# Kernel tuning notes

Hardware: AMD Instinct MI355X
Metric: run time of the kernel (lower is better)

## Reference

```python
import jax, jax.numpy as jnp
import numpy as np
import math

D = 1024
N_HEAD = 16
HEAD_D = D // N_HEAD

def setup_inputs() -> dict:
    key = jax.random.key(0)
    ks = jax.random.split(key, 10)
    b, s = 4, 2048
    scale = 1.0 / math.sqrt(D)
    inp = {
        "decoder_hs": jax.random.normal(ks[0], (b, s, D), dtype=jnp.float32),
        "encoder_hs": jax.random.normal(ks[1], (b, s, D), dtype=jnp.float32),
        "Wq": jax.random.normal(ks[2], (D, D), dtype=jnp.float32) * scale,
        "bq": jnp.zeros((D,), dtype=jnp.float32),
        "Wk": jax.random.normal(ks[3], (D, D), dtype=jnp.float32) * scale,
        "bk": jnp.zeros((D,), dtype=jnp.float32),
        "Wv": jax.random.normal(ks[4], (D, D), dtype=jnp.float32) * scale,
        "bv": jnp.zeros((D,), dtype=jnp.float32),
        "Wp": jax.random.normal(ks[5], (D, D), dtype=jnp.float32) * scale,
        "bp": jnp.zeros((D,), dtype=jnp.float32),
    }
    return inp

def _split_heads(x, b, s):
    # [b, s, d] -> [b, n_head, s, head_d]
    return x.reshape(b, s, N_HEAD, HEAD_D).transpose(0, 2, 1, 3)

def reference(decoder_hs, encoder_hs, Wq, bq, Wk, bk, Wv, bv, Wp, bp):
    b, s, d = decoder_hs.shape
    # torch nn.Linear: y = x @ W.T + b
    q = _split_heads(decoder_hs @ Wq.T + bq, b, s)
    k = _split_heads(encoder_hs @ Wk.T + bk, b, s)
    v = _split_heads(encoder_hs @ Wv.T + bv, b, s)
    att = jnp.einsum('bhqd,bhkd->bhqk', q, k) * (1.0 / math.sqrt(HEAD_D))
    att = jax.nn.softmax(att, axis=-1)  # mask is None, dropout = 0 (eval)
    y = jnp.einsum('bhqk,bhkd->bhqd', att, v)
    y = y.transpose(0, 2, 1, 3).reshape(b, s, d)
    return y @ Wp.T + bp
```

## Files before the change

kernel.cpp:

```cpp
#include <hip/hip_runtime.h>
#include <hip/hip_bf16.h>

typedef __attribute__((ext_vector_type(8))) short bf16x8;
typedef __attribute__((ext_vector_type(4))) float floatx4;
typedef __attribute__((ext_vector_type(16))) float floatx16;
typedef __attribute__((ext_vector_type(2))) int int2v;

#define MFMA_16x16x32(A, B, C) __builtin_amdgcn_mfma_f32_16x16x32_bf16(A, B, C, 0, 0, 0)
#define MFMA_32x32x16(A, B, C) __builtin_amdgcn_mfma_f32_32x32x16_bf16(A, B, C, 0, 0, 0)

__device__ __forceinline__ unsigned short f2b(float f) {
    __hip_bfloat16 h = __float2bfloat16(f);
    unsigned short u;
    __builtin_memcpy(&u, &h, 2);
    return u;
}
__device__ __forceinline__ unsigned pk2(float a, float b) {
    __hip_bfloat162 h = __float22bfloat162_rn(float2{a, b});
    unsigned u;
    __builtin_memcpy(&u, &h, 4);
    return u;
}
__device__ __forceinline__ bf16x8 mk8(int a, int b, int c, int d) {
    union { int u[4]; bf16x8 v; } x;
    x.u[0] = a; x.u[1] = b; x.u[2] = c; x.u[3] = d;
    return x.v;
}
__device__ __forceinline__ void async_lds16(const void* g, void* l) {
    __builtin_amdgcn_global_load_lds((__attribute__((address_space(1))) void*)g,
                                     (__attribute__((address_space(3))) void*)l, 16, 0, 0);
}

struct CvtArgs {
    const float* src[6];
    unsigned short* dst[6];
    float scale[6];
    int n8[6];
};
__global__ __launch_bounds__(256) void convert_kernel(CvtArgs a) {
    const int t = blockIdx.y;
    const int i = blockIdx.x * 256 + threadIdx.x;
    if (i >= a.n8[t]) return;
    const float sc = a.scale[t];
    const float4* s = (const float4*)a.src[t];
    const float4 x = s[2 * i], y = s[2 * i + 1];
    bf16x8 v;
    v[0] = (short)f2b(x.x * sc); v[1] = (short)f2b(x.y * sc);
    v[2] = (short)f2b(x.z * sc); v[3] = (short)f2b(x.w * sc);
    v[4] = (short)f2b(y.x * sc); v[5] = (short)f2b(y.y * sc);
    v[6] = (short)f2b(y.z * sc); v[7] = (short)f2b(y.w * sc);
    *(bf16x8*)(a.dst[t] + (size_t)i * 8) = v;
}

struct QKVArgs {
    const unsigned short* A[3];
    const unsigned short* B[3];
    const float* bias[3];
    float bscale[3];
    unsigned short* C[3];
};
__global__ __launch_bounds__(256, 4) void gemm_qkv(QKVArgs args) {
    constexpr int M = 8192, N = 1024, K = 1024;
    __shared__ __align__(16) unsigned short As[2][4096];
    __shared__ __align__(16) unsigned short Bs[2][4096];

    const int z = blockIdx.z;
    const unsigned short* __restrict__ A = args.A[z];
    const unsigned short* __restrict__ B = args.B[z];
    const float* __restrict__ bias = args.bias[z];
    const float bsc = args.bscale[z];
    unsigned short* __restrict__ C = args.C[z];

    const int tid  = threadIdx.x;
    const int wave = tid >> 6;
    const int lane = tid & 63;
    const int l16  = lane & 15;
    const int quad = lane >> 4;
    const int bm = (blockIdx.x & 63) * 128;
    const int bn = (blockIdx.x >> 6) * 128;
    const int wm = (wave >> 1) * 64;
    const int wn = (wave & 1) * 64;

    const int srow = tid >> 2;
    const int skb  = (((tid & 3) ^ ((tid >> 2) & 3) ^ ((tid >> 4) & 3)) * 8);
    const int cq   = ((quad ^ (l16 & 3) ^ ((l16 >> 2) & 3)) * 8);

    floatx4 acc[4][4] = {};

    auto stage = [&](int buf, int k0) {
        async_lds16(A + (size_t)(bm + srow) * K + skb + k0,      &As[buf][tid * 8]);
        async_lds16(A + (size_t)(bm + 64 + srow) * K + skb + k0, &As[buf][2048 + tid * 8]);
        async_lds16(B + (size_t)(bn + srow) * K + skb + k0,      &Bs[buf][tid * 8]);
        async_lds16(B + (size_t)(bn + 64 + srow) * K + skb + k0, &Bs[buf][2048 + tid * 8]);
    };

    stage(0, 0);
    for (int it = 0; it < K / 32; ++it) {
        __syncthreads();
        if (it + 1 < K / 32) stage((it + 1) & 1, (it + 1) * 32);
        const unsigned short* Ac = &As[it & 1][0];
        const unsigned short* Bc = &Bs[it & 1][0];

        bf16x8 af[4], bfr[4];
        #pragma unroll
        for (int i = 0; i < 4; ++i)
            af[i] = *(const bf16x8*)&Ac[(wm + i * 16 + l16) * 32 + cq];
        #pragma unroll
        for (int j = 0; j < 4; ++j)
            bfr[j] = *(const bf16x8*)&Bc[(wn + j * 16 + l16) * 32 + cq];
        #pragma unroll
        for (int i = 0; i < 4; ++i)
            #pragma unroll
            for (int j = 0; j < 4; ++j)
                acc[i][j] = MFMA_16x16x32(af[i], bfr[j], acc[i][j]);
    }

    if (z == 2) {
        #pragma unroll
        for (int j = 0; j < 4; ++j) {
            const int col = bn + wn + j * 16 + l16;
            const float bv = bias[col] * bsc;
            #pragma unroll
            for (int i = 0; i < 4; ++i) {
                uint2 w;
                w.x = pk2(acc[i][j][0] + bv, acc[i][j][1] + bv);
                w.y = pk2(acc[i][j][2] + bv, acc[i][j][3] + bv);
                const size_t off = (size_t)col * (size_t)M + (bm + wm + i * 16 + quad * 4);
                *(uint2*)&C[off] = w;
            }
        }
    } else {
        #pragma unroll
        for (int i = 0; i < 4; ++i) {
            const int row = bm + wm + i * 16 + quad * 4;
            #pragma unroll
            for (int j = 0; j < 4; ++j) {
                const int col = bn + wn + j * 16 + l16;
                const float bv = bias[col] * bsc;
                #pragma unroll
                for (int r = 0; r < 4; ++r)
                    C[(size_t)(row + r) * N + col] = f2b(acc[i][j][r] + bv);
            }
        }
    }
}

__global__ __launch_bounds__(256, 4) void gemm_out(
    const unsigned short* __restrict__ A, const unsigned short* __restrict__ B,
    const float* __restrict__ bias, float* __restrict__ C,
    int M, int N, int K)
{
    __shared__ __align__(16) unsigned short As[2][4096];
    __shared__ __align__(16) unsigned short Bs[2][4096];

    const int tid  = threadIdx.x;
    const int wave = tid >> 6;
    const int lane = tid & 63;
    const int l16  = lane & 15;
    const int quad = lane >> 4;
    const int bm = (blockIdx.x & 63) * 128;
    const int bn = (blockIdx.x >> 6) * 128;
    const int wm = (wave >> 1) * 64;
    const int wn = (wave & 1) * 64;

    const int srow = tid >> 2;
    const int skb  = (((tid & 3) ^ ((tid >> 2) & 3) ^ ((tid >> 4) & 3)) * 8);
    const int cq   = ((quad ^ (l16 & 3) ^ ((l16 >> 2) & 3)) * 8);

    floatx4 acc[4][4] = {};

    auto stage = [&](int buf, int k0) {
        async_lds16(A + (size_t)(bm + srow) * K + skb + k0,      &As[buf][tid * 8]);
        async_lds16(A + (size_t)(bm + 64 + srow) * K + skb + k0, &As[buf][2048 + tid * 8]);
        async_lds16(B + (size_t)(bn + srow) * K + skb + k0,      &Bs[buf][tid * 8]);
        async_lds16(B + (size_t)(bn + 64 + srow) * K + skb + k0, &Bs[buf][2048 + tid * 8]);
    };

    stage(0, 0);
    for (int it = 0; it < K / 32; ++it) {
        __syncthreads();
        if (it + 1 < K / 32) stage((it + 1) & 1, (it + 1) * 32);
        const unsigned short* Ac = &As[it & 1][0];
        const unsigned short* Bc = &Bs[it & 1][0];

        bf16x8 af[4], bfr[4];
        #pragma unroll
        for (int i = 0; i < 4; ++i)
            af[i] = *(const bf16x8*)&Ac[(wm + i * 16 + l16) * 32 + cq];
        #pragma unroll
        for (int j = 0; j < 4; ++j)
            bfr[j] = *(const bf16x8*)&Bc[(wn + j * 16 + l16) * 32 + cq];
        #pragma unroll
        for (int i = 0; i < 4; ++i)
            #pragma unroll
            for (int j = 0; j < 4; ++j)
                acc[i][j] = MFMA_16x16x32(af[i], bfr[j], acc[i][j]);
    }

    float* Tw = ((wave < 2) ? (float*)&As[0][0] : (float*)&Bs[0][0]) + (wave & 1) * 1024;
    const int rrow = lane >> 2;
    const int rch  = lane & 3;
    #pragma unroll
    for (int i = 0; i < 4; ++i) {
        #pragma unroll
        for (int j = 0; j < 4; ++j) {
            const int col = j * 16 + l16;
            const float bv = bias[bn + wn + col];
            floatx4 v;
            #pragma unroll
            for (int r = 0; r < 4; ++r) v[r] = acc[i][j][r] + bv;
            *(floatx4*)&Tw[col * 16 + ((quad ^ (col & 3)) << 2)] = v;
        }
        const int grow = bm + wm + i * 16 + rrow;
        #pragma unroll
        for (int k = 0; k < 4; ++k) {
            const int c0 = (rch + 4 * k) * 4;
            floatx4 v;
            #pragma unroll
            for (int c = 0; c < 4; ++c) {
                const int col = c0 + c;
                v[c] = Tw[col * 16 + ((((rrow >> 2) ^ col) & 3) << 2) + (rrow & 3)];
            }
            *(floatx4*)&C[(size_t)grow * N + bn + wn + c0] = v;
        }
    }
}

__global__ __launch_bounds__(256, 4) void attn_kernel(
    const unsigned short* __restrict__ Q, const unsigned short* __restrict__ Kg,
    const unsigned short* __restrict__ Vt, unsigned short* __restrict__ Y)
{
    __shared__ __align__(16) unsigned short Ks[2][4096];
    __shared__ __align__(16) unsigned short Vs[2][4096];

    const int tid  = threadIdx.x;
    const int wave = tid >> 6;
    const int lane = tid & 63;
    const int l31  = lane & 31;
    const int hi   = lane >> 5;
    const int x7   = lane & 7;
    const int h4   = ((lane >> 4) & 1) << 2;
    const int bh = blockIdx.x & 63;
    const int qt = blockIdx.x >> 6;
    const int b  = bh >> 4;
    const int h  = bh & 15;
    const int q0 = qt * 128 + wave * 32;
    const size_t base  = ((size_t)b * 2048) * 1024 + (size_t)h * 64;
    const size_t vbase = ((size_t)h * 64) * 8192 + (size_t)b * 2048;

    bf16x8 qf[4];
    {
        const size_t qrow = base + (size_t)(q0 + l31) * 1024 + hi * 8;
        #pragma unroll
        for (int ks = 0; ks < 4; ++ks)
            qf[ks] = *(const bf16x8*)&Q[qrow + ks * 16];
    }

    bf16x8 ones;
    #pragma unroll
    for (int e = 0; e < 8; ++e) ones[e] = (short)0x3F80;
    const floatx16 Z16 = {0.f,0.f,0.f,0.f,0.f,0.f,0.f,0.f,
                          0.f,0.f,0.f,0.f,0.f,0.f,0.f,0.f};

    floatx16 o0 = Z16, o1 = Z16;
    floatx16 rs = Z16;

    const int r0  = tid >> 3;
    const int csw = (tid & 7) ^ (r0 & 7) ^ (((tid >> 7) & 1) << 2);

    int co[4];
    #pragma unroll
    for (int ks = 0; ks < 4; ++ks) co[ks] = (((ks * 2 + hi) ^ x7 ^ h4) * 8);
    const int krow = l31 * 64;

    auto stage = [&](int buf, int kv0) {
        async_lds16(&Kg[base + (size_t)(kv0 + r0) * 1024 + csw * 8],      &Ks[buf][tid * 8]);
        async_lds16(&Kg[base + (size_t)(kv0 + 32 + r0) * 1024 + csw * 8], &Ks[buf][2048 + tid * 8]);
        async_lds16(&Vt[vbase + (size_t)r0 * 8192 + kv0 + csw * 8],        &Vs[buf][tid * 8]);
        async_lds16(&Vt[vbase + (size_t)(r0 + 32) * 8192 + kv0 + csw * 8], &Vs[buf][2048 + tid * 8]);
    };

    auto procP = [&](const floatx16& st, bf16x8& paA, bf16x8& paB) {
        float e[16];
        #pragma unroll
        for (int i = 0; i < 16; ++i) e[i] = __builtin_amdgcn_exp2f(st[i]);
        const int w0 = (int)pk2(e[0],  e[1]);
        const int w1 = (int)pk2(e[2],  e[3]);
        const int w2 = (int)pk2(e[4],  e[5]);
        const int w3 = (int)pk2(e[6],  e[7]);
        const int w4 = (int)pk2(e[8],  e[9]);
        const int w5 = (int)pk2(e[10], e[11]);
        const int w6 = (int)pk2(e[12], e[13]);
        const int w7 = (int)pk2(e[14], e[15]);
        const int2v a0 = __builtin_amdgcn_permlane32_swap(w0, w2, false, false);
        const int2v a1 = __builtin_amdgcn_permlane32_swap(w1, w3, false, false);
        const int2v a2 = __builtin_amdgcn_permlane32_swap(w4, w6, false, false);
        const int2v a3 = __builtin_amdgcn_permlane32_swap(w5, w7, false, false);
        paA = mk8(a0.x, a1.x, a0.y, a1.y);
        paB = mk8(a2.x, a3.x, a2.y, a3.y);
    };

    stage(0, 0);
    for (int t = 0; t < 32; ++t) {
        __syncthreads();
        if (t < 31) stage((t + 1) & 1, (t + 1) * 64);
        const unsigned short* Kc = &Ks[t & 1][0];
        const unsigned short* Vc = &Vs[t & 1][0];

        floatx16 st0 = Z16, st1 = Z16;
        __builtin_amdgcn_s_setprio(1);
        #pragma unroll
        for (int ks = 0; ks < 4; ++ks) {
            const bf16x8 kf0 = *(const bf16x8*)&Kc[krow + co[ks]];
            const bf16x8 kf1 = *(const bf16x8*)&Kc[2048 + krow + co[ks]];
            st0 = MFMA_32x32x16(kf0, qf[ks], st0);
            st1 = MFMA_32x32x16(kf1, qf[ks], st1);
        }
        __builtin_amdgcn_s_setprio(0);

        bf16x8 pa[4];
        procP(st0, pa[0], pa[1]);
        procP(st1, pa[2], pa[3]);

        __builtin_amdgcn_s_setprio(1);
        #pragma unroll
        for (int f = 0; f < 4; ++f) {
            const bf16x8 v0 = *(const bf16x8*)&Vc[krow + co[f]];
            const bf16x8 v1 = *(const bf16x8*)&Vc[2048 + krow + co[f]];
            o0 = MFMA_32x32x16(pa[f], v0, o0);
            o1 = MFMA_32x32x16(pa[f], v1, o1);
            rs = MFMA_32x32x16(pa[f], ones, rs);
        }
        __builtin_amdgcn_s_setprio(0);
    }

    #pragma unroll
    for (int g = 0; g < 4; ++g) {
        #pragma unroll
        for (int e2 = 0; e2 < 4; ++e2) {
            const int reg = g * 4 + e2;
            const float inv = 1.0f / rs[reg];
            const size_t row = q0 + 8 * g + 4 * hi + e2;
            Y[base + row * 1024 + l31]      = f2b(o0[reg] * inv);
            Y[base + row * 1024 + 32 + l31] = f2b(o1[reg] * inv);
        }
    }
}

extern "C" void kernel_launch(void* const* d_in, const int* in_sizes, int n_in,
                              void* d_out, int out_size, void* d_ws, size_t ws_size,
                              hipStream_t stream)
{
    const float* dec = (const float*)d_in[0];
    const float* enc = (const float*)d_in[1];
    const float* Wq  = (const float*)d_in[2];
    const float* bq  = (const float*)d_in[3];
    const float* Wk  = (const float*)d_in[4];
    const float* bk  = (const float*)d_in[5];
    const float* Wv  = (const float*)d_in[6];
    const float* bv  = (const float*)d_in[7];
    const float* Wp  = (const float*)d_in[8];
    const float* bp  = (const float*)d_in[9];

    const size_t NTOK = 8192, DM = 1024;
    unsigned short* ws = (unsigned short*)d_ws;
    unsigned short* decB = ws;
    unsigned short* encB = decB + NTOK * DM;
    unsigned short* WqB  = encB + NTOK * DM;
    unsigned short* WkB  = WqB + DM * DM;
    unsigned short* WvB  = WkB + DM * DM;
    unsigned short* WpB  = WvB + DM * DM;
    unsigned short* Qb   = WpB + DM * DM;
    unsigned short* Kb   = Qb + NTOK * DM;
    unsigned short* VtG  = Kb + NTOK * DM;
    unsigned short* Yb   = VtG + NTOK * DM;

    const float C_SM = 0.18033688f;

    CvtArgs a;
    a.src[0] = dec; a.src[1] = enc; a.src[2] = Wq; a.src[3] = Wk; a.src[4] = Wv; a.src[5] = Wp;
    a.dst[0] = decB; a.dst[1] = encB; a.dst[2] = WqB; a.dst[3] = WkB; a.dst[4] = WvB; a.dst[5] = WpB;
    a.scale[0] = 1.f; a.scale[1] = 1.f; a.scale[2] = C_SM;
    a.scale[3] = 1.f; a.scale[4] = 1.f; a.scale[5] = 1.f;
    a.n8[0] = a.n8[1] = (int)(NTOK * DM / 8);
    a.n8[2] = a.n8[3] = a.n8[4] = a.n8[5] = (int)(DM * DM / 8);
    convert_kernel<<<dim3(4096, 6), 256, 0, stream>>>(a);

    QKVArgs qa;
    qa.A[0] = decB; qa.A[1] = encB; qa.A[2] = encB;
    qa.B[0] = WqB;  qa.B[1] = WkB;  qa.B[2] = WvB;
    qa.bias[0] = bq; qa.bias[1] = bk; qa.bias[2] = bv;
    qa.bscale[0] = C_SM; qa.bscale[1] = 1.f; qa.bscale[2] = 1.f;
    qa.C[0] = Qb;   qa.C[1] = Kb;   qa.C[2] = VtG;
    gemm_qkv<<<dim3(512, 1, 3), 256, 0, stream>>>(qa);

    attn_kernel<<<dim3(1024), 256, 0, stream>>>(Qb, Kb, VtG, Yb);
    gemm_out<<<dim3(512), 256, 0, stream>>>(Yb, WpB, bp, (float*)d_out, 8192, 1024, 1024);
}
```

Before: 325.4 us.

## Process two query sub-tiles per wave in attention to reuse K/V fragments

Each wave now handles 64 query rows instead of 32, holding two sets of Q fragments and accumulators. Every K and V fragment loaded from LDS feeds twice as many MFMAs, and the block count halves, so each block covers 256 queries and K/V staging traffic per query drops. The trade-off is higher register pressure: launch bounds fall from 4 to 2 blocks per CU, with fewer blocks and less occupancy to hide the exp/softmax latency.

```diff
diff --git a/kernel.cpp b/kernel.cpp
--- a/kernel.cpp
+++ b/kernel.cpp
@@ -226,7 +226,7 @@
     }
 }
 
-__global__ __launch_bounds__(256, 4) void attn_kernel(
+__global__ __launch_bounds__(256, 2) void attn_kernel(
     const unsigned short* __restrict__ Q, const unsigned short* __restrict__ Kg,
     const unsigned short* __restrict__ Vt, unsigned short* __restrict__ Y)
 {
@@ -244,16 +244,17 @@
     const int qt = blockIdx.x >> 6;
     const int b  = bh >> 4;
     const int h  = bh & 15;
-    const int q0 = qt * 128 + wave * 32;
+    const int q0 = qt * 256 + wave * 64;
     const size_t base  = ((size_t)b * 2048) * 1024 + (size_t)h * 64;
     const size_t vbase = ((size_t)h * 64) * 8192 + (size_t)b * 2048;
 
-    bf16x8 qf[4];
-    {
-        const size_t qrow = base + (size_t)(q0 + l31) * 1024 + hi * 8;
+    bf16x8 qf[2][4];
+    #pragma unroll
+    for (int qb = 0; qb < 2; ++qb) {
+        const size_t qrow = base + (size_t)(q0 + qb * 32 + l31) * 1024 + hi * 8;
         #pragma unroll
         for (int ks = 0; ks < 4; ++ks)
-            qf[ks] = *(const bf16x8*)&Q[qrow + ks * 16];
+            qf[qb][ks] = *(const bf16x8*)&Q[qrow + ks * 16];
     }
 
     bf16x8 ones;
@@ -262,8 +263,8 @@
     const floatx16 Z16 = {0.f,0.f,0.f,0.f,0.f,0.f,0.f,0.f,
                           0.f,0.f,0.f,0.f,0.f,0.f,0.f,0.f};
 
-    floatx16 o0 = Z16, o1 = Z16;
-    floatx16 rs = Z16;
+    floatx16 o[2][2] = {{Z16, Z16}, {Z16, Z16}};
+    floatx16 rs[2]   = {Z16, Z16};
 
     const int r0  = tid >> 3;
     const int csw = (tid & 7) ^ (r0 & 7) ^ (((tid >> 7) & 1) << 2);
@@ -307,42 +308,52 @@
         const unsigned short* Kc = &Ks[t & 1][0];
         const unsigned short* Vc = &Vs[t & 1][0];
 
-        floatx16 st0 = Z16, st1 = Z16;
+        floatx16 st[2][2] = {{Z16, Z16}, {Z16, Z16}};
         __builtin_amdgcn_s_setprio(1);
         #pragma unroll
         for (int ks = 0; ks < 4; ++ks) {
             const bf16x8 kf0 = *(const bf16x8*)&Kc[krow + co[ks]];
             const bf16x8 kf1 = *(const bf16x8*)&Kc[2048 + krow + co[ks]];
-            st0 = MFMA_32x32x16(kf0, qf[ks], st0);
-            st1 = MFMA_32x32x16(kf1, qf[ks], st1);
+            st[0][0] = MFMA_32x32x16(kf0, qf[0][ks], st[0][0]);
+            st[0][1] = MFMA_32x32x16(kf0, qf[1][ks], st[0][1]);
+            st[1][0] = MFMA_32x32x16(kf1, qf[0][ks], st[1][0]);
+            st[1][1] = MFMA_32x32x16(kf1, qf[1][ks], st[1][1]);
         }
         __builtin_amdgcn_s_setprio(0);
 
-        bf16x8 pa[4];
-        procP(st0, pa[0], pa[1]);
-        procP(st1, pa[2], pa[3]);
+        bf16x8 pa[4][2];
+        procP(st[0][0], pa[0][0], pa[1][0]);
+        procP(st[0][1], pa[0][1], pa[1][1]);
+        procP(st[1][0], pa[2][0], pa[3][0]);
+        procP(st[1][1], pa[2][1], pa[3][1]);
 
         __builtin_amdgcn_s_setprio(1);
         #pragma unroll
         for (int f = 0; f < 4; ++f) {
             const bf16x8 v0 = *(const bf16x8*)&Vc[krow + co[f]];
             const bf16x8 v1 = *(const bf16x8*)&Vc[2048 + krow + co[f]];
-            o0 = MFMA_32x32x16(pa[f], v0, o0);
-            o1 = MFMA_32x32x16(pa[f], v1, o1);
-            rs = MFMA_32x32x16(pa[f], ones, rs);
+            #pragma unroll
+            for (int qb = 0; qb < 2; ++qb) {
+                o[qb][0] = MFMA_32x32x16(pa[f][qb], v0, o[qb][0]);
+                o[qb][1] = MFMA_32x32x16(pa[f][qb], v1, o[qb][1]);
+                rs[qb]   = MFMA_32x32x16(pa[f][qb], ones, rs[qb]);
+            }
         }
         __builtin_amdgcn_s_setprio(0);
     }
 
     #pragma unroll
-    for (int g = 0; g < 4; ++g) {
-        #pragma unroll
-        for (int e2 = 0; e2 < 4; ++e2) {
-            const int reg = g * 4 + e2;
-            const float inv = 1.0f / rs[reg];
-            const size_t row = q0 + 8 * g + 4 * hi + e2;
-            Y[base + row * 1024 + l31]      = f2b(o0[reg] * inv);
-            Y[base + row * 1024 + 32 + l31] = f2b(o1[reg] * inv);
+    for (int qb = 0; qb < 2; ++qb) {
+        #pragma unroll
+        for (int g = 0; g < 4; ++g) {
+            #pragma unroll
+            for (int e2 = 0; e2 < 4; ++e2) {
+                const int reg = g * 4 + e2;
+                const float inv = 1.0f / rs[qb][reg];
+                const size_t row = q0 + qb * 32 + 8 * g + 4 * hi + e2;
+                Y[base + row * 1024 + l31]      = f2b(o[qb][0][reg] * inv);
+                Y[base + row * 1024 + 32 + l31] = f2b(o[qb][1][reg] * inv);
+            }
         }
     }
 }
@@ -394,6 +405,6 @@
     qa.C[0] = Qb;   qa.C[1] = Kb;   qa.C[2] = VtG;
     gemm_qkv<<<dim3(512, 1, 3), 256, 0, stream>>>(qa);
 
-    attn_kernel<<<dim3(1024), 256, 0, stream>>>(Qb, Kb, VtG, Yb);
+    attn_kernel<<<dim3(512), 256, 0, stream>>>(Qb, Kb, VtG, Yb);
     gemm_out<<<dim3(512), 256, 0, stream>>>(Yb, WpB, bp, (float*)d_out, 8192, 1024, 1024);
 }
```

New measurement: 309.7 us (median of 3 runs). -4.8%, faster.
